# Optimization experiments

Hardware: AMD Instinct MI355X
Metric: run time of the kernel (lower is better)

Reference implementation:

```python
import jax, jax.numpy as jnp
import numpy as np

RANK = 256
ORDER = 3
B = 8192
NODES_PER = 9
NMAP = 5 ** 6          # 15625 dnn-key nodes
NDD = NMAP + 1         # + 1 device node
MDD = 2048             # edges into device node
POW5 = jnp.array([5**5, 5**4, 5**3, 5**2, 5, 1], dtype=jnp.int32)


def sage_gcn(x, src, dst, n, W, b):
    # DGL SAGEConv(aggregator='gcn'): h = fc((sum_in_neighbors + self) / (in_deg + 1))
    agg = jax.ops.segment_sum(x[src], dst, num_segments=n)
    deg = jax.ops.segment_sum(jnp.ones((src.shape[0],), x.dtype), dst, num_segments=n)
    h = (agg + x) / (deg + 1.0)[:, None]
    return h @ W + b


def layernorm(x, g, b, eps=1e-5):
    m = x.mean(-1, keepdims=True)
    v = ((x - m) ** 2).mean(-1, keepdims=True)
    return (x - m) * jax.lax.rsqrt(v + eps) * g + b


def setup_inputs() -> dict:
    key = jax.random.key(0)
    ks = jax.random.split(key, 10)
    rng = np.random.default_rng(0)
    # batched DNN graphs: B bidirectional 9-node chains
    base = np.arange(B, dtype=np.int32)[:, None] * NODES_PER
    s = (base + np.arange(NODES_PER - 1, dtype=np.int32)[None, :]).ravel()
    d = s + 1
    edge_src = jnp.asarray(np.concatenate([s, d]))
    edge_dst = jnp.asarray(np.concatenate([d, s]))
    # unique key tuples (base-5 digits of unique dnn indices)
    key_idx = rng.choice(NMAP, size=B, replace=False).astype(np.int32)
    digits = np.stack([(key_idx // 5 ** (5 - j)) % 5 for j in range(6)], axis=1)
    key_ids = jnp.asarray(digits, dtype=jnp.int32)
    features = jax.random.randint(ks[0], (B, NODES_PER), 0, 6, dtype=jnp.int32)
    dd_src = jnp.asarray(rng.choice(NMAP, size=MDD, replace=False).astype(np.int32))

    r = RANK
    def gn(k, shape, scale=0.02):
        return jax.random.normal(k, shape, jnp.float32) * scale

    return dict(
        features=features, key_ids=key_ids,
        edge_src=edge_src, edge_dst=edge_dst, dd_src=dd_src,
        emb=gn(ks[1], (6, r)),
        sage_W=gn(ks[2], (ORDER, r, r)), sage_b=jnp.zeros((ORDER, r)),
        ln_g=jnp.ones((ORDER, r)), ln_b=jnp.zeros((ORDER, r)),
        dd_W=gn(ks[3], (r, r)), dd_b=jnp.zeros((r,)),
        norm_g=jnp.ones((r,)), norm_b=jnp.zeros((r,)),
        info_W=gn(ks[4], (5, r)), info_b=jnp.zeros((r,)),
        aug_data=gn(ks[5], (1, 5), 1.0),
        pred_W1=gn(ks[6], (2 * r, r)), pred_b1=jnp.zeros((r,)),
        pred_W2=gn(ks[7], (r, 1)), pred_b2=jnp.zeros((1,)),
    )


def reference(features, key_ids, edge_src, edge_dst, dd_src,
              emb, sage_W, sage_b, ln_g, ln_b,
              dd_W, dd_b, norm_g, norm_b,
              info_W, info_b, aug_data,
              pred_W1, pred_b1, pred_W2, pred_b2):
    n = B * NODES_PER
    # GraphReader: embed + ORDER x (SAGEConv-gcn -> LayerNorm -> ReLU)
    feats = emb[features].reshape(n, RANK)
    for i in range(ORDER):
        feats = sage_gcn(feats, edge_src, edge_dst, n, sage_W[i], sage_b[i])
        feats = jax.nn.relu(layernorm(feats, ln_g[i], ln_b[i]))
    # first node of each 9-node sub-graph
    graph_embeds = feats.reshape(B, NODES_PER, RANK)[:, 0]  # [B, r]

    # scatter graph embeddings into the dnn-device graph node features
    key_idx = (key_ids * POW5).sum(axis=1)  # base-5 index from 6-tuple
    dd = jnp.zeros((NDD, RANK), feats.dtype).at[key_idx].set(graph_embeds)
    info = aug_data @ info_W + info_b  # [1, r]
    dd = dd.at[NDD - 1].set(info[0])

    # SAGEConv-gcn on the dnn-device graph (all edges point at the device node)
    dd_dst = jnp.full_like(dd_src, NDD - 1)
    dd = sage_gcn(dd, dd_src, dd_dst, NDD, dd_W, dd_b)
    dd = jax.nn.relu(layernorm(dd, norm_g, norm_b))

    info_embeds = jnp.broadcast_to(dd[-1], (B, RANK))
    embeds = jnp.concatenate([graph_embeds, info_embeds], axis=1)  # [B, 2r]
    h = jax.nn.relu(embeds @ pred_W1 + pred_b1)
    return h @ pred_W2 + pred_b2  # [B, 1]
```

## Files before the change

### kernel.cpp

```cpp
#include <hip/hip_runtime.h>

#define RANK 256
#define NB 8192
#define NMAP 15625

typedef unsigned short ushort_t;
typedef short  mfma_ab __attribute__((ext_vector_type(8)));
typedef float  f32x4   __attribute__((ext_vector_type(4)));

#define GEH_OFF   0
#define GEL_OFF   4194304
#define WTH_OFF   8388608
#define WTL_OFF   8912896
#define INV_OFF   9437184
#define PARTS_OFF 9499712
#define C2_OFF    9630784

#define DD_BLOCKS 128

__device__ __forceinline__ float b2f(ushort_t u) {
    return __uint_as_float(((unsigned)u) << 16);
}
__device__ __forceinline__ ushort_t f2b(float f) {
    unsigned u = __float_as_uint(f);
    return (ushort_t)((u + 0x7FFFu + ((u >> 16) & 1u)) >> 16);
}

__device__ __forceinline__ f32x4 mfma_bf16(mfma_ab a, mfma_ab b, f32x4 c) {
#if defined(__gfx950__)
    return __builtin_amdgcn_mfma_f32_16x16x32_bf16(a, b, c, 0, 0, 0);
#else
    (void)a; (void)b;
    return c;
#endif
}

__global__ void k_init_inv(int* inv) {
    int i = blockIdx.x * 256 + threadIdx.x;
    if (i < NMAP) inv[i] = -1;
}

__global__ void k_scatter(const int* key_ids, int* inv) {
    int b = blockIdx.x * 256 + threadIdx.x;
    const int* kp = key_ids + b * 6;
    int k = kp[0]*3125 + kp[1]*625 + kp[2]*125 + kp[3]*25 + kp[4]*5 + kp[5];
    inv[k] = b;
}

__global__ void k_prep_w(const float* __restrict__ sageW,
                         const float* __restrict__ predW1,
                         ushort_t* __restrict__ WTh,
                         ushort_t* __restrict__ WTl)
{
    const int id = blockIdx.x;
    const int mat = id >> 4, tile = id & 15;
    const int tr = tile >> 2, tc = tile & 3;
    const float* src = (mat < 3) ? (sageW + mat * 65536) : predW1;
    ushort_t* dh = WTh + mat * 65536;
    ushort_t* dl = WTl + mat * 65536;
    __shared__ float t[64][65];
    const int tid = threadIdx.x;
    const int c = tid & 63, r0 = tid >> 6;
    #pragma unroll
    for (int i = 0; i < 16; ++i) {
        int r = r0 + i * 4;
        t[r][c] = src[(tr*64 + r) * 256 + tc*64 + c];
    }
    __syncthreads();
    #pragma unroll
    for (int i = 0; i < 16; ++i) {
        int r = r0 + i * 4;
        float f = t[c][r];
        ushort_t h = f2b(f);
        dh[(tc*64 + r) * 256 + tr*64 + c] = h;
        dl[(tc*64 + r) * 256 + tr*64 + c] = f2b(f - b2f(h));
    }
}

#define GR_G 5
#define GR_RPAD 48
#define XP 260
#define AP 264


#define AGG_LOAD(IT, V)                                                        \
    {                                                                          \
        const int t_ = tid + (IT) * 512;                                       \
        const int row_ = t_ >> 6, c4_ = t_ & 63;                               \
        V = make_float4(0.f, 0.f, 0.f, 0.f);                                   \
        if (row_ < nreal) {                                                    \
            const int j_ = row_ % 9;                                           \
            V = *(const float4*)(sXf + row_ * XP + c4_ * 4);                   \
            float cnt_ = 1.f;                                                  \
            if (j_ > 0) {                                                      \
                float4 u_ = *(const float4*)(sXf + (row_ - 1) * XP + c4_ * 4); \
                V.x += u_.x; V.y += u_.y; V.z += u_.z; V.w += u_.w; cnt_ += 1.f;\
            }                                                                  \
            if (j_ < 8) {                                                      \
                float4 u_ = *(const float4*)(sXf + (row_ + 1) * XP + c4_ * 4); \
                V.x += u_.x; V.y += u_.y; V.z += u_.z; V.w += u_.w; cnt_ += 1.f;\
            }                                                                  \
            const float sc_ = 1.0f / cnt_;                                     \
            V.x *= sc_; V.y *= sc_; V.z *= sc_; V.w *= sc_;                    \
        }                                                                      \
    }

#define AGG_STORE(IT, V)                                                       \
    {                                                                          \
        const int t_ = tid + (IT) * 512;                                       \
        const int row_ = t_ >> 6, c4_ = t_ & 63;                               \
        const ushort_t h0_ = f2b(V.x), h1_ = f2b(V.y);                         \
        const ushort_t h2_ = f2b(V.z), h3_ = f2b(V.w);                         \
        const ushort_t l0_ = f2b(V.x - b2f(h0_)), l1_ = f2b(V.y - b2f(h1_));   \
        const ushort_t l2_ = f2b(V.z - b2f(h2_)), l3_ = f2b(V.w - b2f(h3_));   \
        *(uint2*)(sAh + row_ * AP + c4_ * 4) =                                 \
            make_uint2((unsigned)h0_ | ((unsigned)h1_ << 16),                  \
                       (unsigned)h2_ | ((unsigned)h3_ << 16));                 \
        *(uint2*)(sAl + row_ * AP + c4_ * 4) =                                 \
            make_uint2((unsigned)l0_ | ((unsigned)l1_ << 16),                  \
                       (unsigned)l2_ | ((unsigned)l3_ << 16));                 \
    }

#define LN_PART(ACC0, ACC1, MT)                                                \
    _Pragma("unroll")                                                          \
    for (int q = 0; q < 4; ++q) {                                              \
        ACC0[q] += bias0; ACC1[q] += bias1;                                    \
        float s_  = ACC0[q] + ACC1[q];                                         \
        float ss_ = ACC0[q] * ACC0[q] + ACC1[q] * ACC1[q];                     \
        _Pragma("unroll")                                                      \
        for (int mask = 1; mask <= 8; mask <<= 1) {                            \
            s_  += __shfl_xor(s_, mask, 64);                                   \
            ss_ += __shfl_xor(ss_, mask, 64);                                  \
        }                                                                      \
        if (l15 == 0) sPart[(MT) * 16 + q4 * 4 + q][wid] = make_float2(s_, ss_);\
    }

#define LN_WRITE(ACC0, ACC1, MT)                                               \
    _Pragma("unroll")                                                          \
    for (int q = 0; q < 4; ++q) {                                              \
        const int row_ = (MT) * 16 + q4 * 4 + q;                               \
        const float2 mr_ = sMV[row_];                                          \
        float v0_ = (ACC0[q] - mr_.x) * mr_.y * gv0 + bv0;                     \
        float v1_ = (ACC1[q] - mr_.x) * mr_.y * gv1 + bv1;                     \
        v0_ = fmaxf(v0_, 0.f); v1_ = fmaxf(v1_, 0.f);                          \
        if (L < 2) {                                                           \
            sXf[row_ * XP + colb + l15]      = v0_;                            \
            sXf[row_ * XP + colb + 16 + l15] = v1_;                            \
        } else if (row_ < nreal && (row_ % 9) == 0) {                          \
            const int gi_ = row_ / 9;                                          \
            const ushort_t h0_ = f2b(v0_), h1_ = f2b(v1_);                     \
            GEh[(b0 + gi_) * RANK + colb + l15]      = h0_;                    \
            GEl[(b0 + gi_) * RANK + colb + l15]      = f2b(v0_ - b2f(h0_));    \
            GEh[(b0 + gi_) * RANK + colb + 16 + l15] = h1_;                    \
            GEl[(b0 + gi_) * RANK + colb + 16 + l15] = f2b(v1_ - b2f(h1_));    \
        }                                                                      \
    }

__global__ __launch_bounds__(512, 4) void k_graph_reader(
    const int* __restrict__ features,
    const float* __restrict__ emb,
    const ushort_t* __restrict__ WTh,
    const ushort_t* __restrict__ WTl,
    const float* __restrict__ sageB,
    const float* __restrict__ lnG,
    const float* __restrict__ lnB,
    ushort_t* __restrict__ GEh,
    ushort_t* __restrict__ GEl)
{
    __shared__ __align__(16) char uLDS[50688];
    float*    sXf = (float*)uLDS;
    ushort_t* sAh = (ushort_t*)uLDS;
    ushort_t* sAl = (ushort_t*)(uLDS + 25344);
    __shared__ float2 sPart[GR_RPAD][8];
    __shared__ float2 sMV[GR_RPAD];
    __shared__ int sFeat[GR_RPAD];

    const int tid  = threadIdx.x;
    const int wid  = tid >> 6;
    const int lane = tid & 63;
    const int q4   = lane >> 4;
    const int l15  = lane & 15;
    const int colb = wid * 32;

    const int b0    = blockIdx.x * GR_G;
    const int ngr   = min(GR_G, NB - b0);
    const int nreal = ngr * 9;

    if (tid < GR_RPAD) sFeat[tid] = (tid < nreal) ? features[b0 * 9 + tid] : 0;
    __syncthreads();

    #pragma unroll
    for (int it = 0; it < 6; ++it) {
        int t = tid + it * 512;
        int row = t >> 6, c4 = t & 63;
        if (row < nreal)
            *(float4*)(sXf + row * XP + c4 * 4) =
                *(const float4*)(emb + sFeat[row] * RANK + c4 * 4);
    }

    const f32x4 vzero = {0.f, 0.f, 0.f, 0.f};

    for (int L = 0; L < 3; ++L) {
        float bias0, bias1, gv0, gv1, bv0, bv1;
        {
            int col0 = colb + l15, col1 = colb + 16 + l15;
            bias0 = sageB[L * RANK + col0]; bias1 = sageB[L * RANK + col1];
            gv0   = lnG[L * RANK + col0];   gv1   = lnG[L * RANK + col1];
            bv0   = lnB[L * RANK + col0];   bv1   = lnB[L * RANK + col1];
        }
        __syncthreads();

        float4 a0, a1, a2, a3, a4, a5;
        AGG_LOAD(0, a0) AGG_LOAD(1, a1) AGG_LOAD(2, a2)
        AGG_LOAD(3, a3) AGG_LOAD(4, a4) AGG_LOAD(5, a5)
        __syncthreads();

        AGG_STORE(0, a0) AGG_STORE(1, a1) AGG_STORE(2, a2)
        AGG_STORE(3, a3) AGG_STORE(4, a4) AGG_STORE(5, a5)
        __syncthreads();

        f32x4 acc00 = vzero, acc01 = vzero;
        f32x4 acc10 = vzero, acc11 = vzero;
        f32x4 acc20 = vzero, acc21 = vzero;
        const ushort_t* bh = WTh + L * 65536 + (colb + l15) * RANK + q4 * 8;
        const ushort_t* bl = WTl + L * 65536 + (colb + l15) * RANK + q4 * 8;
        #pragma unroll
        for (int ks = 0; ks < 8; ++ks) {
            mfma_ab B0h = *(const mfma_ab*)(bh + ks * 32);
            mfma_ab B0l = *(const mfma_ab*)(bl + ks * 32);
            mfma_ab B1h = *(const mfma_ab*)(bh + 16 * RANK + ks * 32);
            mfma_ab B1l = *(const mfma_ab*)(bl + 16 * RANK + ks * 32);
            const int ab = l15 * AP + ks * 32 + q4 * 8;

            mfma_ab A0h = *(const mfma_ab*)(sAh + ab);
            mfma_ab A0l = *(const mfma_ab*)(sAl + ab);
            acc00 = mfma_bf16(A0h, B0h, acc00);
            acc00 = mfma_bf16(A0l, B0h, acc00);
            acc00 = mfma_bf16(A0h, B0l, acc00);
            acc01 = mfma_bf16(A0h, B1h, acc01);
            acc01 = mfma_bf16(A0l, B1h, acc01);
            acc01 = mfma_bf16(A0h, B1l, acc01);

            mfma_ab A1h = *(const mfma_ab*)(sAh + ab + 16 * AP);
            mfma_ab A1l = *(const mfma_ab*)(sAl + ab + 16 * AP);
            acc10 = mfma_bf16(A1h, B0h, acc10);
            acc10 = mfma_bf16(A1l, B0h, acc10);
            acc10 = mfma_bf16(A1h, B0l, acc10);
            acc11 = mfma_bf16(A1h, B1h, acc11);
            acc11 = mfma_bf16(A1l, B1h, acc11);
            acc11 = mfma_bf16(A1h, B1l, acc11);

            mfma_ab A2h = *(const mfma_ab*)(sAh + ab + 32 * AP);
            mfma_ab A2l = *(const mfma_ab*)(sAl + ab + 32 * AP);
            acc20 = mfma_bf16(A2h, B0h, acc20);
            acc20 = mfma_bf16(A2l, B0h, acc20);
            acc20 = mfma_bf16(A2h, B0l, acc20);
            acc21 = mfma_bf16(A2h, B1h, acc21);
            acc21 = mfma_bf16(A2l, B1h, acc21);
            acc21 = mfma_bf16(A2h, B1l, acc21);
        }

        LN_PART(acc00, acc01, 0)
        LN_PART(acc10, acc11, 1)
        LN_PART(acc20, acc21, 2)
        __syncthreads();

        if (tid < GR_RPAD) {
            float s = 0.f, q = 0.f;
            #pragma unroll
            for (int w = 0; w < 8; ++w) { float2 p = sPart[tid][w]; s += p.x; q += p.y; }
            float m = s * (1.0f / 256.0f);
            float var = q * (1.0f / 256.0f) - m * m;
            if (var < 0.f) var = 0.f;
            sMV[tid] = make_float2(m, rsqrtf(var + 1e-5f));
        }
        __syncthreads();

        LN_WRITE(acc00, acc01, 0)
        LN_WRITE(acc10, acc11, 1)
        LN_WRITE(acc20, acc21, 2)
    }
}

__global__ void k_dd_agg(const int* __restrict__ dd_src,
                         const int* __restrict__ inv,
                         const ushort_t* __restrict__ GEh,
                         const ushort_t* __restrict__ GEl,
                         float* __restrict__ parts)
{
    const int c  = threadIdx.x;
    const int e0 = blockIdx.x * (2048 / DD_BLOCKS);
    float s = 0.f;
    for (int e = e0; e < e0 + (2048 / DD_BLOCKS); ++e) {
        int b = inv[dd_src[e]];
        if (b >= 0) s += b2f(GEh[b * RANK + c]) + b2f(GEl[b * RANK + c]);
    }
    parts[blockIdx.x * RANK + c] = s;
}

__global__ void k_device(const float* __restrict__ parts,
                         const float* __restrict__ aug,
                         const float* __restrict__ infoW,
                         const float* __restrict__ infoB,
                         const float* __restrict__ ddW,
                         const float* __restrict__ ddB,
                         const float* __restrict__ normG,
                         const float* __restrict__ normB,
                         const float* __restrict__ predW1,
                         const float* __restrict__ predB1,
                         float* __restrict__ c2)
{
    __shared__ float sh[RANK];
    __shared__ float sdev[RANK];
    __shared__ float sred[RANK];
    const int n = threadIdx.x;

    float agg = 0.f;
    for (int p = 0; p < DD_BLOCKS; ++p) agg += parts[p * RANK + n];
    float info = infoB[n];
    for (int j = 0; j < 5; ++j) info += aug[j] * infoW[j * RANK + n];
    sh[n] = (agg + info) * (1.0f / 2049.0f);
    __syncthreads();

    float y = ddB[n];
    for (int k = 0; k < RANK; ++k) y += sh[k] * ddW[k * RANK + n];

    sred[n] = y; __syncthreads();
    for (int off = 128; off > 0; off >>= 1) {
        if (n < off) sred[n] += sred[n + off];
        __syncthreads();
    }
    float s = sred[0]; __syncthreads();
    sred[n] = y * y; __syncthreads();
    for (int off = 128; off > 0; off >>= 1) {
        if (n < off) sred[n] += sred[n + off];
        __syncthreads();
    }
    float q = sred[0]; __syncthreads();

    float m = s * (1.0f / 256.0f);
    float var = q * (1.0f / 256.0f) - m * m;
    if (var < 0.f) var = 0.f;
    float rs = rsqrtf(var + 1e-5f);
    float dev = (y - m) * rs * normG[n] + normB[n];
    if (dev < 0.f) dev = 0.f;
    sdev[n] = dev;
    __syncthreads();

    float o = predB1[n];
    for (int k = 0; k < RANK; ++k) o += sdev[k] * predW1[(RANK + k) * RANK + n];
    c2[n] = o;
}

__global__ void k_pred(const ushort_t* __restrict__ GEh,
                       const ushort_t* __restrict__ GEl,
                       const ushort_t* __restrict__ W1h,
                       const ushort_t* __restrict__ W1l,
                       const float* __restrict__ c2,
                       const float* __restrict__ predW2,
                       const float* __restrict__ predB2,
                       float* __restrict__ out)
{
    const int lane = threadIdx.x;
    const int q4 = lane >> 4, l15 = lane & 15;
    const int m0 = blockIdx.x * 16;

    f32x4 acc[16];
    const f32x4 vzero = {0.f, 0.f, 0.f, 0.f};
    #pragma unroll
    for (int Nt = 0; Nt < 16; ++Nt) acc[Nt] = vzero;

    const ushort_t* ah = GEh + (m0 + l15) * RANK + q4 * 8;
    const ushort_t* al = GEl + (m0 + l15) * RANK + q4 * 8;
    const ushort_t* bh = W1h + l15 * RANK + q4 * 8;
    const ushort_t* bl = W1l + l15 * RANK + q4 * 8;
    #pragma unroll
    for (int ks = 0; ks < 8; ++ks) {
        mfma_ab Ah = *(const mfma_ab*)(ah + ks * 32);
        mfma_ab Al = *(const mfma_ab*)(al + ks * 32);
        #pragma unroll
        for (int Nt = 0; Nt < 16; ++Nt) {
            mfma_ab Bh = *(const mfma_ab*)(bh + Nt * 16 * RANK + ks * 32);
            mfma_ab Bl = *(const mfma_ab*)(bl + Nt * 16 * RANK + ks * 32);
            acc[Nt] = mfma_bf16(Ah, Bh, acc[Nt]);
            acc[Nt] = mfma_bf16(Al, Bh, acc[Nt]);
            acc[Nt] = mfma_bf16(Ah, Bl, acc[Nt]);
        }
    }

    float op0 = 0.f, op1 = 0.f, op2 = 0.f, op3 = 0.f;
    #pragma unroll
    for (int Nt = 0; Nt < 16; ++Nt) {
        int col = Nt * 16 + l15;
        float c2v = c2[col];
        float w2v = predW2[col];
        float h0 = fmaxf(acc[Nt][0] + c2v, 0.f);
        float h1 = fmaxf(acc[Nt][1] + c2v, 0.f);
        float h2 = fmaxf(acc[Nt][2] + c2v, 0.f);
        float h3 = fmaxf(acc[Nt][3] + c2v, 0.f);
        op0 += h0 * w2v; op1 += h1 * w2v; op2 += h2 * w2v; op3 += h3 * w2v;
    }
    #pragma unroll
    for (int mask = 1; mask <= 8; mask <<= 1) {
        op0 += __shfl_xor(op0, mask, 64);
        op1 += __shfl_xor(op1, mask, 64);
        op2 += __shfl_xor(op2, mask, 64);
        op3 += __shfl_xor(op3, mask, 64);
    }
    if (l15 == 0) {
        float b2 = predB2[0];
        out[m0 + q4 * 4 + 0] = op0 + b2;
        out[m0 + q4 * 4 + 1] = op1 + b2;
        out[m0 + q4 * 4 + 2] = op2 + b2;
        out[m0 + q4 * 4 + 3] = op3 + b2;
    }
}

extern "C" void kernel_launch(void* const* d_in, const int* in_sizes, int n_in,
                              void* d_out, int out_size, void* d_ws, size_t ws_size,
                              hipStream_t stream) {
    const int* features  = (const int*)d_in[0];
    const int* key_ids   = (const int*)d_in[1];
    const int* dd_src    = (const int*)d_in[4];
    const float* emb     = (const float*)d_in[5];
    const float* sageW   = (const float*)d_in[6];
    const float* sageB   = (const float*)d_in[7];
    const float* lnG     = (const float*)d_in[8];
    const float* lnB     = (const float*)d_in[9];
    const float* ddW     = (const float*)d_in[10];
    const float* ddB     = (const float*)d_in[11];
    const float* normG   = (const float*)d_in[12];
    const float* normB   = (const float*)d_in[13];
    const float* infoW   = (const float*)d_in[14];
    const float* infoB   = (const float*)d_in[15];
    const float* aug     = (const float*)d_in[16];
    const float* predW1  = (const float*)d_in[17];
    const float* predB1  = (const float*)d_in[18];
    const float* predW2  = (const float*)d_in[19];
    const float* predB2  = (const float*)d_in[20];

    char* ws = (char*)d_ws;
    ushort_t* GEh   = (ushort_t*)(ws + GEH_OFF);
    ushort_t* GEl   = (ushort_t*)(ws + GEL_OFF);
    ushort_t* WTh   = (ushort_t*)(ws + WTH_OFF);
    ushort_t* WTl   = (ushort_t*)(ws + WTL_OFF);
    int*      inv   = (int*)(ws + INV_OFF);
    float*    parts = (float*)(ws + PARTS_OFF);
    float*    c2    = (float*)(ws + C2_OFF);
    float*    outp  = (float*)d_out;

    k_init_inv<<<62, 256, 0, stream>>>(inv);
    k_scatter<<<32, 256, 0, stream>>>(key_ids, inv);
    k_prep_w<<<64, 256, 0, stream>>>(sageW, predW1, WTh, WTl);
    k_graph_reader<<<(NB + GR_G - 1) / GR_G, 512, 0, stream>>>(
        features, emb, WTh, WTl, sageB, lnG, lnB, GEh, GEl);
    k_dd_agg<<<DD_BLOCKS, 256, 0, stream>>>(dd_src, inv, GEh, GEl, parts);
    k_device<<<1, 256, 0, stream>>>(parts, aug, infoW, infoB, ddW, ddB,
                                    normG, normB, predW1, predB1, c2);
    k_pred<<<NB / 16, 64, 0, stream>>>(GEh, GEl, WTh + 3 * 65536, WTl + 3 * 65536,
                                       c2, predW2, predB2, outp);
}
```

Before: 395.1 us.

## Shrink graph-reader blocks to 3 graphs and retile pred GEMM across two waves

The graph reader now processes 3 graphs (27 rows, padded to 32) per block instead of 5, dropping the third MFMA row tile. It also replaces the aliased LDS union with separate fp32 and bf16 buffers, which lets the aggregation and split-store happen in one pass without an extra barrier. The prediction kernel becomes 2 waves per block covering 32 rows, each wave handling 128 output columns with two row tiles that reuse the same B loads, and the partial sums are combined through shared memory. The intent is more blocks and better occupancy in the reader, and more reuse of the W1 loads in the pred GEMM, at the cost of more blocks and an extra reduction step.

```diff
diff --git a/kernel.cpp b/kernel.cpp
--- a/kernel.cpp
+++ b/kernel.cpp
@@ -77,49 +77,10 @@
     }
 }
 
-#define GR_G 5
-#define GR_RPAD 48
+#define GR_G 3
+#define GR_RPAD 32
 #define XP 260
 #define AP 264
-
-
-#define AGG_LOAD(IT, V)                                                        \
-    {                                                                          \
-        const int t_ = tid + (IT) * 512;                                       \
-        const int row_ = t_ >> 6, c4_ = t_ & 63;                               \
-        V = make_float4(0.f, 0.f, 0.f, 0.f);                                   \
-        if (row_ < nreal) {                                                    \
-            const int j_ = row_ % 9;                                           \
-            V = *(const float4*)(sXf + row_ * XP + c4_ * 4);                   \
-            float cnt_ = 1.f;                                                  \
-            if (j_ > 0) {                                                      \
-                float4 u_ = *(const float4*)(sXf + (row_ - 1) * XP + c4_ * 4); \
-                V.x += u_.x; V.y += u_.y; V.z += u_.z; V.w += u_.w; cnt_ += 1.f;\
-            }                                                                  \
-            if (j_ < 8) {                                                      \
-                float4 u_ = *(const float4*)(sXf + (row_ + 1) * XP + c4_ * 4); \
-                V.x += u_.x; V.y += u_.y; V.z += u_.z; V.w += u_.w; cnt_ += 1.f;\
-            }                                                                  \
-            const float sc_ = 1.0f / cnt_;                                     \
-            V.x *= sc_; V.y *= sc_; V.z *= sc_; V.w *= sc_;                    \
-        }                                                                      \
-    }
-
-#define AGG_STORE(IT, V)                                                       \
-    {                                                                          \
-        const int t_ = tid + (IT) * 512;                                       \
-        const int row_ = t_ >> 6, c4_ = t_ & 63;                               \
-        const ushort_t h0_ = f2b(V.x), h1_ = f2b(V.y);                         \
-        const ushort_t h2_ = f2b(V.z), h3_ = f2b(V.w);                         \
-        const ushort_t l0_ = f2b(V.x - b2f(h0_)), l1_ = f2b(V.y - b2f(h1_));   \
-        const ushort_t l2_ = f2b(V.z - b2f(h2_)), l3_ = f2b(V.w - b2f(h3_));   \
-        *(uint2*)(sAh + row_ * AP + c4_ * 4) =                                 \
-            make_uint2((unsigned)h0_ | ((unsigned)h1_ << 16),                  \
-                       (unsigned)h2_ | ((unsigned)h3_ << 16));                 \
-        *(uint2*)(sAl + row_ * AP + c4_ * 4) =                                 \
-            make_uint2((unsigned)l0_ | ((unsigned)l1_ << 16),                  \
-                       (unsigned)l2_ | ((unsigned)l3_ << 16));                 \
-    }
 
 #define LN_PART(ACC0, ACC1, MT)                                                \
     _Pragma("unroll")                                                          \
@@ -139,20 +100,22 @@
     _Pragma("unroll")                                                          \
     for (int q = 0; q < 4; ++q) {                                              \
         const int row_ = (MT) * 16 + q4 * 4 + q;                               \
-        const float2 mr_ = sMV[row_];                                          \
-        float v0_ = (ACC0[q] - mr_.x) * mr_.y * gv0 + bv0;                     \
-        float v1_ = (ACC1[q] - mr_.x) * mr_.y * gv1 + bv1;                     \
-        v0_ = fmaxf(v0_, 0.f); v1_ = fmaxf(v1_, 0.f);                          \
-        if (L < 2) {                                                           \
-            sXf[row_ * XP + colb + l15]      = v0_;                            \
-            sXf[row_ * XP + colb + 16 + l15] = v1_;                            \
-        } else if (row_ < nreal && (row_ % 9) == 0) {                          \
-            const int gi_ = row_ / 9;                                          \
-            const ushort_t h0_ = f2b(v0_), h1_ = f2b(v1_);                     \
-            GEh[(b0 + gi_) * RANK + colb + l15]      = h0_;                    \
-            GEl[(b0 + gi_) * RANK + colb + l15]      = f2b(v0_ - b2f(h0_));    \
-            GEh[(b0 + gi_) * RANK + colb + 16 + l15] = h1_;                    \
-            GEl[(b0 + gi_) * RANK + colb + 16 + l15] = f2b(v1_ - b2f(h1_));    \
+        if (row_ < nreal) {                                                    \
+            const float2 mr_ = sMV[row_];                                      \
+            float v0_ = (ACC0[q] - mr_.x) * mr_.y * gv0 + bv0;                 \
+            float v1_ = (ACC1[q] - mr_.x) * mr_.y * gv1 + bv1;                 \
+            v0_ = fmaxf(v0_, 0.f); v1_ = fmaxf(v1_, 0.f);                      \
+            if (L < 2) {                                                       \
+                sXf[row_ * XP + colb + l15]      = v0_;                        \
+                sXf[row_ * XP + colb + 16 + l15] = v1_;                        \
+            } else if ((row_ % 9) == 0) {                                      \
+                const int gi_ = row_ / 9;                                      \
+                const ushort_t h0_ = f2b(v0_), h1_ = f2b(v1_);                 \
+                GEh[(b0 + gi_) * RANK + colb + l15]      = h0_;                \
+                GEl[(b0 + gi_) * RANK + colb + l15]      = f2b(v0_ - b2f(h0_));\
+                GEh[(b0 + gi_) * RANK + colb + 16 + l15] = h1_;                \
+                GEl[(b0 + gi_) * RANK + colb + 16 + l15] = f2b(v1_ - b2f(h1_));\
+            }                                                                  \
         }                                                                      \
     }
 
@@ -167,10 +130,9 @@
     ushort_t* __restrict__ GEh,
     ushort_t* __restrict__ GEl)
 {
-    __shared__ __align__(16) char uLDS[50688];
-    float*    sXf = (float*)uLDS;
-    ushort_t* sAh = (ushort_t*)uLDS;
-    ushort_t* sAl = (ushort_t*)(uLDS + 25344);
+    __shared__ __align__(16) float    sXf[27 * XP];
+    __shared__ __align__(16) ushort_t sAh[GR_RPAD * AP];
+    __shared__ __align__(16) ushort_t sAl[GR_RPAD * AP];
     __shared__ float2 sPart[GR_RPAD][8];
     __shared__ float2 sMV[GR_RPAD];
     __shared__ int sFeat[GR_RPAD];
@@ -185,17 +147,19 @@
     const int b0    = blockIdx.x * GR_G;
     const int ngr   = min(GR_G, NB - b0);
     const int nreal = ngr * 9;
+    const int ntask = nreal * 64;
 
     if (tid < GR_RPAD) sFeat[tid] = (tid < nreal) ? features[b0 * 9 + tid] : 0;
     __syncthreads();
 
     #pragma unroll
-    for (int it = 0; it < 6; ++it) {
+    for (int it = 0; it < 4; ++it) {
         int t = tid + it * 512;
-        int row = t >> 6, c4 = t & 63;
-        if (row < nreal)
+        if (t < ntask) {
+            int row = t >> 6, c4 = t & 63;
             *(float4*)(sXf + row * XP + c4 * 4) =
                 *(const float4*)(emb + sFeat[row] * RANK + c4 * 4);
+        }
     }
 
     const f32x4 vzero = {0.f, 0.f, 0.f, 0.f};
@@ -210,18 +174,38 @@
         }
         __syncthreads();
 
-        float4 a0, a1, a2, a3, a4, a5;
-        AGG_LOAD(0, a0) AGG_LOAD(1, a1) AGG_LOAD(2, a2)
-        AGG_LOAD(3, a3) AGG_LOAD(4, a4) AGG_LOAD(5, a5)
-        __syncthreads();
-
-        AGG_STORE(0, a0) AGG_STORE(1, a1) AGG_STORE(2, a2)
-        AGG_STORE(3, a3) AGG_STORE(4, a4) AGG_STORE(5, a5)
-        __syncthreads();
-
-        f32x4 acc00 = vzero, acc01 = vzero;
-        f32x4 acc10 = vzero, acc11 = vzero;
-        f32x4 acc20 = vzero, acc21 = vzero;
+        #pragma unroll
+        for (int it = 0; it < 4; ++it) {
+            int t = tid + it * 512;
+            if (t < ntask) {
+                int row = t >> 6, c4 = t & 63;
+                int j = row % 9;
+                float4 v = *(const float4*)(sXf + row * XP + c4 * 4);
+                float cnt = 1.f;
+                if (j > 0) {
+                    float4 u = *(const float4*)(sXf + (row - 1) * XP + c4 * 4);
+                    v.x += u.x; v.y += u.y; v.z += u.z; v.w += u.w; cnt += 1.f;
+                }
+                if (j < 8) {
+                    float4 u = *(const float4*)(sXf + (row + 1) * XP + c4 * 4);
+                    v.x += u.x; v.y += u.y; v.z += u.z; v.w += u.w; cnt += 1.f;
+                }
+                float sc = 1.0f / cnt;
+                v.x *= sc; v.y *= sc; v.z *= sc; v.w *= sc;
+                ushort_t h0 = f2b(v.x), h1 = f2b(v.y), h2 = f2b(v.z), h3 = f2b(v.w);
+                ushort_t l0 = f2b(v.x - b2f(h0)), l1 = f2b(v.y - b2f(h1));
+                ushort_t l2 = f2b(v.z - b2f(h2)), l3 = f2b(v.w - b2f(h3));
+                *(uint2*)(sAh + row * AP + c4 * 4) =
+                    make_uint2((unsigned)h0 | ((unsigned)h1 << 16),
+                               (unsigned)h2 | ((unsigned)h3 << 16));
+                *(uint2*)(sAl + row * AP + c4 * 4) =
+                    make_uint2((unsigned)l0 | ((unsigned)l1 << 16),
+                               (unsigned)l2 | ((unsigned)l3 << 16));
+            }
+        }
+        __syncthreads();
+
+        f32x4 acc00 = vzero, acc01 = vzero, acc10 = vzero, acc11 = vzero;
         const ushort_t* bh = WTh + L * 65536 + (colb + l15) * RANK + q4 * 8;
         const ushort_t* bl = WTl + L * 65536 + (colb + l15) * RANK + q4 * 8;
         #pragma unroll
@@ -249,20 +233,10 @@
             acc11 = mfma_bf16(A1h, B1h, acc11);
             acc11 = mfma_bf16(A1l, B1h, acc11);
             acc11 = mfma_bf16(A1h, B1l, acc11);
-
-            mfma_ab A2h = *(const mfma_ab*)(sAh + ab + 32 * AP);
-            mfma_ab A2l = *(const mfma_ab*)(sAl + ab + 32 * AP);
-            acc20 = mfma_bf16(A2h, B0h, acc20);
-            acc20 = mfma_bf16(A2l, B0h, acc20);
-            acc20 = mfma_bf16(A2h, B0l, acc20);
-            acc21 = mfma_bf16(A2h, B1h, acc21);
-            acc21 = mfma_bf16(A2l, B1h, acc21);
-            acc21 = mfma_bf16(A2h, B1l, acc21);
         }
 
         LN_PART(acc00, acc01, 0)
         LN_PART(acc10, acc11, 1)
-        LN_PART(acc20, acc21, 2)
         __syncthreads();
 
         if (tid < GR_RPAD) {
@@ -278,7 +252,6 @@
 
         LN_WRITE(acc00, acc01, 0)
         LN_WRITE(acc10, acc11, 1)
-        LN_WRITE(acc20, acc21, 2)
     }
 }
 
@@ -352,68 +325,98 @@
     c2[n] = o;
 }
 
-__global__ void k_pred(const ushort_t* __restrict__ GEh,
-                       const ushort_t* __restrict__ GEl,
-                       const ushort_t* __restrict__ W1h,
-                       const ushort_t* __restrict__ W1l,
-                       const float* __restrict__ c2,
-                       const float* __restrict__ predW2,
-                       const float* __restrict__ predB2,
-                       float* __restrict__ out)
+#define PRED_MFMA3(ACC, AH, AL, BH, BL)                                        \
+    ACC = mfma_bf16(AH, BH, ACC);                                              \
+    ACC = mfma_bf16(AL, BH, ACC);                                              \
+    ACC = mfma_bf16(AH, BL, ACC);
+
+#define PRED_N(NT, C0, C1)                                                     \
+    {                                                                          \
+        mfma_ab Bh_ = *(const mfma_ab*)(bh + (NT) * 16 * RANK + ks * 32);      \
+        mfma_ab Bl_ = *(const mfma_ab*)(bl + (NT) * 16 * RANK + ks * 32);      \
+        PRED_MFMA3(C0, A0h, A0l, Bh_, Bl_)                                     \
+        PRED_MFMA3(C1, A1h, A1l, Bh_, Bl_)                                     \
+    }
+
+#define PRED_EPI(NT, C0, C1)                                                   \
+    {                                                                          \
+        const int col_ = colb + (NT) * 16 + l15;                               \
+        const float c2v_ = c2[col_], w2v_ = predW2[col_];                      \
+        op00 += fmaxf(C0[0] + c2v_, 0.f) * w2v_;                               \
+        op01 += fmaxf(C0[1] + c2v_, 0.f) * w2v_;                               \
+        op02 += fmaxf(C0[2] + c2v_, 0.f) * w2v_;                               \
+        op03 += fmaxf(C0[3] + c2v_, 0.f) * w2v_;                               \
+        op10 += fmaxf(C1[0] + c2v_, 0.f) * w2v_;                               \
+        op11 += fmaxf(C1[1] + c2v_, 0.f) * w2v_;                               \
+        op12 += fmaxf(C1[2] + c2v_, 0.f) * w2v_;                               \
+        op13 += fmaxf(C1[3] + c2v_, 0.f) * w2v_;                               \
+    }
+
+__global__ __launch_bounds__(128, 4) void k_pred(
+    const ushort_t* __restrict__ GEh,
+    const ushort_t* __restrict__ GEl,
+    const ushort_t* __restrict__ W1h,
+    const ushort_t* __restrict__ W1l,
+    const float* __restrict__ c2,
+    const float* __restrict__ predW2,
+    const float* __restrict__ predB2,
+    float* __restrict__ out)
 {
-    const int lane = threadIdx.x;
+    __shared__ float sO[2][32];
+    const int tid = threadIdx.x;
+    const int wid = tid >> 6;
+    const int lane = tid & 63;
     const int q4 = lane >> 4, l15 = lane & 15;
-    const int m0 = blockIdx.x * 16;
-
-    f32x4 acc[16];
+    const int colb = wid * 128;
+    const int m0 = blockIdx.x * 32;
+
     const f32x4 vzero = {0.f, 0.f, 0.f, 0.f};
-    #pragma unroll
-    for (int Nt = 0; Nt < 16; ++Nt) acc[Nt] = vzero;
-
-    const ushort_t* ah = GEh + (m0 + l15) * RANK + q4 * 8;
-    const ushort_t* al = GEl + (m0 + l15) * RANK + q4 * 8;
-    const ushort_t* bh = W1h + l15 * RANK + q4 * 8;
-    const ushort_t* bl = W1l + l15 * RANK + q4 * 8;
+    f32x4 c00 = vzero, c01 = vzero, c02 = vzero, c03 = vzero;
+    f32x4 c04 = vzero, c05 = vzero, c06 = vzero, c07 = vzero;
+    f32x4 c10 = vzero, c11 = vzero, c12 = vzero, c13 = vzero;
+    f32x4 c14 = vzero, c15 = vzero, c16 = vzero, c17 = vzero;
+
+    const ushort_t* ah0 = GEh + (m0 + l15) * RANK + q4 * 8;
+    const ushort_t* al0 = GEl + (m0 + l15) * RANK + q4 * 8;
+    const ushort_t* ah1 = ah0 + 16 * RANK;
+    const ushort_t* al1 = al0 + 16 * RANK;
+    const ushort_t* bh = W1h + (colb + l15) * RANK + q4 * 8;
+    const ushort_t* bl = W1l + (colb + l15) * RANK + q4 * 8;
+
     #pragma unroll
     for (int ks = 0; ks < 8; ++ks) {
-        mfma_ab Ah = *(const mfma_ab*)(ah + ks * 32);
-        mfma_ab Al = *(const mfma_ab*)(al + ks * 32);
-        #pragma unroll
-        for (int Nt = 0; Nt < 16; ++Nt) {
-            mfma_ab Bh = *(const mfma_ab*)(bh + Nt * 16 * RANK + ks * 32);
-            mfma_ab Bl = *(const mfma_ab*)(bl + Nt * 16 * RANK + ks * 32);
-            acc[Nt] = mfma_bf16(Ah, Bh, acc[Nt]);
-            acc[Nt] = mfma_bf16(Al, Bh, acc[Nt]);
-            acc[Nt] = mfma_bf16(Ah, Bl, acc[Nt]);
-        }
-    }
-
-    float op0 = 0.f, op1 = 0.f, op2 = 0.f, op3 = 0.f;
-    #pragma unroll
-    for (int Nt = 0; Nt < 16; ++Nt) {
-        int col = Nt * 16 + l15;
-        float c2v = c2[col];
-        float w2v = predW2[col];
-        float h0 = fmaxf(acc[Nt][0] + c2v, 0.f);
-        float h1 = fmaxf(acc[Nt][1] + c2v, 0.f);
-        float h2 = fmaxf(acc[Nt][2] + c2v, 0.f);
-        float h3 = fmaxf(acc[Nt][3] + c2v, 0.f);
-        op0 += h0 * w2v; op1 += h1 * w2v; op2 += h2 * w2v; op3 += h3 * w2v;
-    }
+        mfma_ab A0h = *(const mfma_ab*)(ah0 + ks * 32);
+        mfma_ab A0l = *(const mfma_ab*)(al0 + ks * 32);
+        mfma_ab A1h = *(const mfma_ab*)(ah1 + ks * 32);
+        mfma_ab A1l = *(const mfma_ab*)(al1 + ks * 32);
+        PRED_N(0, c00, c10) PRED_N(1, c01, c11)
+        PRED_N(2, c02, c12) PRED_N(3, c03, c13)
+        PRED_N(4, c04, c14) PRED_N(5, c05, c15)
+        PRED_N(6, c06, c16) PRED_N(7, c07, c17)
+    }
+
+    float op00 = 0.f, op01 = 0.f, op02 = 0.f, op03 = 0.f;
+    float op10 = 0.f, op11 = 0.f, op12 = 0.f, op13 = 0.f;
+    PRED_EPI(0, c00, c10) PRED_EPI(1, c01, c11)
+    PRED_EPI(2, c02, c12) PRED_EPI(3, c03, c13)
+    PRED_EPI(4, c04, c14) PRED_EPI(5, c05, c15)
+    PRED_EPI(6, c06, c16) PRED_EPI(7, c07, c17)
+
     #pragma unroll
     for (int mask = 1; mask <= 8; mask <<= 1) {
-        op0 += __shfl_xor(op0, mask, 64);
-        op1 += __shfl_xor(op1, mask, 64);
-        op2 += __shfl_xor(op2, mask, 64);
-        op3 += __shfl_xor(op3, mask, 64);
+        op00 += __shfl_xor(op00, mask, 64); op01 += __shfl_xor(op01, mask, 64);
+        op02 += __shfl_xor(op02, mask, 64); op03 += __shfl_xor(op03, mask, 64);
+        op10 += __shfl_xor(op10, mask, 64); op11 += __shfl_xor(op11, mask, 64);
+        op12 += __shfl_xor(op12, mask, 64); op13 += __shfl_xor(op13, mask, 64);
     }
     if (l15 == 0) {
-        float b2 = predB2[0];
-        out[m0 + q4 * 4 + 0] = op0 + b2;
-        out[m0 + q4 * 4 + 1] = op1 + b2;
-        out[m0 + q4 * 4 + 2] = op2 + b2;
-        out[m0 + q4 * 4 + 3] = op3 + b2;
-    }
+        sO[wid][q4 * 4 + 0] = op00; sO[wid][q4 * 4 + 1] = op01;
+        sO[wid][q4 * 4 + 2] = op02; sO[wid][q4 * 4 + 3] = op03;
+        sO[wid][16 + q4 * 4 + 0] = op10; sO[wid][16 + q4 * 4 + 1] = op11;
+        sO[wid][16 + q4 * 4 + 2] = op12; sO[wid][16 + q4 * 4 + 3] = op13;
+    }
+    __syncthreads();
+    if (tid < 32) out[m0 + tid] = sO[0][tid] + sO[1][tid] + predB2[0];
 }
 
 extern "C" void kernel_launch(void* const* d_in, const int* in_sizes, int n_in,
@@ -457,6 +460,6 @@
     k_dd_agg<<<DD_BLOCKS, 256, 0, stream>>>(dd_src, inv, GEh, GEl, parts);
     k_device<<<1, 256, 0, stream>>>(parts, aug, infoW, infoB, ddW, ddB,
                                     normG, normB, predW1, predB1, c2);
-    k_pred<<<NB / 16, 64, 0, stream>>>(GEh, GEl, WTh + 3 * 65536, WTl + 3 * 65536,
-                                       c2, predW2, predB2, outp);
-}
+    k_pred<<<NB / 32, 128, 0, stream>>>(GEh, GEl, WTh + 3 * 65536, WTl + 3 * 65536,
+                                        c2, predW2, predB2, outp);
+}
```

New measurement: 436.4 us. +10.5%, slower.
